# Performance work log

Measured on AMD Instinct MI355X. Metric: run time of the kernel, lower is better.

## Reference

```python
import jax, jax.numpy as jnp
import numpy as np

FEATS = 768
HEAD = 12
HD = FEATS // HEAD  # 64
B, N = 128, 197


def setup_inputs() -> dict:
    key = jax.random.key(0)
    k0, k1, k2 = jax.random.split(key, 3)
    x = jax.random.normal(k0, (B, N, FEATS), dtype=jnp.float32)
    W_qkv = jax.random.normal(k1, (HEAD, HD, 3 * HD), dtype=jnp.float32) * 0.05
    b_qkv = jnp.zeros((HEAD, 3 * HD), dtype=jnp.float32)
    # out_dim_3dk: Linear(feats -> feats)
    W_out = jax.random.normal(k2, (FEATS, FEATS), dtype=jnp.float32) * 0.02
    b_out = jnp.zeros((FEATS,), dtype=jnp.float32)
    return {"x": x, "W_qkv": W_qkv, "b_qkv": b_qkv, "W_out": W_out, "b_out": b_out}


def reference(x, W_qkv, b_qkv, W_out, b_out):
    b, n, f = x.shape
    h, hd = W_qkv.shape[0], W_qkv.shape[1]
    # x.chunk(head, dim=2) == reshape into per-head feature slices
    xh = x.reshape(b, n, h, hd)
    # per-head Linear(hd -> 3*hd): hX_dim_3dk
    qkv = jnp.einsum('bnhd,hde->bnhe', xh, W_qkv) + b_qkv  # [b,n,h,3*hd]
    q, k, v = jnp.split(qkv, 3, axis=-1)  # each [b,n,h,hd]
    # NOTE: original scales by sqrt(feats), not sqrt(head_dim)
    scale = jnp.asarray(f, x.dtype) ** 0.5
    scores = jnp.einsum('bihd,bjhd->bhij', q, k) / scale  # [b,h,n,n]
    p = jax.nn.softmax(scores, axis=-1)
    attn = jnp.einsum('bhij,bjhd->bihd', p, v)  # [b,n,h,hd]
    # concat head outputs along feature dim, then out_dim_3dk
    out = attn.reshape(b, n, f) @ W_out + b_out
    return out  # dropout p=0.0 is identity
```

## Files before the change

### kernel.cpp

```cpp
#include <hip/hip_runtime.h>
#include <hip/hip_bf16.h>

#define FEATS 768
#define HEADS 12
#define HD    64
#define BB    128
#define NN    197
#define M_TOT (BB * NN)
#define SCALE_INV (3.6084391824351615e-02f)
#define VS    216

typedef __bf16 bf16x8 __attribute__((ext_vector_type(8)));
typedef float  f32x4  __attribute__((ext_vector_type(4)));
typedef unsigned short u16x8 __attribute__((ext_vector_type(8)));

__device__ __forceinline__ unsigned short f2bf1(float f) {
    __bf16 h = (__bf16)f;
    return *(unsigned short*)&h;
}
__device__ __forceinline__ unsigned int f2bf2(float lo, float hi) {
    return (unsigned int)f2bf1(lo) | ((unsigned int)f2bf1(hi) << 16);
}

__global__ __launch_bounds__(256) void wqkvt_kernel(
    const float* __restrict__ Wqkv, unsigned short* __restrict__ Wt_sw)
{
    __shared__ float wl[64 * 192];
    const int t = threadIdx.x, h = blockIdx.x;
    const float* Wh = Wqkv + (long)h * (64 * 192);
    for (int i = t; i < 64 * 192; i += 256) wl[i] = Wh[i];
    __syncthreads();
    for (int c = t; c < 1536; c += 256) {
        int row = c >> 3, kc = (c & 7) ^ (row & 7);
        u16x8 v;
        #pragma unroll
        for (int j = 0; j < 8; ++j) v[j] = f2bf1(wl[(kc * 8 + j) * 192 + row]);
        *(u16x8*)&Wt_sw[(long)h * 12288 + c * 8] = v;
    }
}

__global__ __launch_bounds__(512, 4) void qkv_attn_fused(
    const float* __restrict__ x, const unsigned short* __restrict__ Wt_sw,
    const float* __restrict__ bqkv, unsigned short* __restrict__ attn)
{
    __shared__ __align__(16) char lds[80912];
    unsigned short* As  = (unsigned short*)lds;
    unsigned short* Ws  = (unsigned short*)(lds + 26624);
    unsigned short* Ql  = (unsigned short*)lds;
    unsigned short* Kl  = (unsigned short*)(lds + 26624);
    unsigned short* Vtl = (unsigned short*)(lds + 53248);
    unsigned short* Pl  = (unsigned short*)lds;

    const int t  = threadIdx.x;
    const int w  = t >> 6, l = t & 63;
    const int lr = l & 15, g = l >> 4, g4 = g * 4;
    const int b  = blockIdx.x, h = blockIdx.y;

    {
        const uint4 z = {0, 0, 0, 0};
        #pragma unroll
        for (int it = 0; it < 4; ++it) {
            int idx = it * 512 + t;
            if (idx < 1729) *(uint4*)&Vtl[idx * 8] = z;
        }
    }
    #pragma unroll
    for (int it = 0; it < 4; ++it) {
        int p = it * 512 + t;
        if (p < 1664) {
            int row = p >> 3, kc = (p & 7) ^ (row & 7);
            uint4 pk = {0, 0, 0, 0};
            if (row < NN) {
                const float* src = x + ((long)b * NN + row) * FEATS + h * HD + kc * 8;
                const float4 x0 = *(const float4*)src;
                const float4 x1 = *(const float4*)(src + 4);
                pk.x = f2bf2(x0.x, x0.y); pk.y = f2bf2(x0.z, x0.w);
                pk.z = f2bf2(x1.x, x1.y); pk.w = f2bf2(x1.z, x1.w);
            }
            *(uint4*)&As[p * 8] = pk;
        }
    }
    const unsigned short* Wh = Wt_sw + (long)h * 12288;
    #pragma unroll
    for (int it = 0; it < 3; ++it) {
        const int cb = it * 512 + w * 64;
        __builtin_amdgcn_global_load_lds(
            (const __attribute__((address_space(1))) void*)(Wh + (cb + l) * 8),
            (__attribute__((address_space(3))) void*)(Ws + cb * 8),
            16, 0, 0);
    }
    __syncthreads();

    const int wn0 = (w & 3) * 48;
    const int f0  = (w >> 2) * 7;
    const int nf_ = (w >> 2) ? 6 : 7;

    bf16x8 bfr[3][2];
    #pragma unroll
    for (int ni = 0; ni < 3; ++ni) {
        const int rn = wn0 + ni * 16 + lr;
        #pragma unroll
        for (int ks = 0; ks < 2; ++ks)
            bfr[ni][ks] = *(const bf16x8*)&Ws[(rn * 8 + ((ks * 4 + g) ^ (rn & 7))) * 8];
    }

    f32x4 acc[7][3];
    #pragma unroll
    for (int ni = 0; ni < 3; ++ni) {
        const int e0 = wn0 + ni * 16;
        if (e0 < 128) {
            const f32x4 bq = *(const f32x4*)&bqkv[h * 192 + e0 + g4];
            #pragma unroll
            for (int mi = 0; mi < 7; ++mi) acc[mi][ni] = bq;
        } else {
            const float bq = bqkv[h * 192 + e0 + lr];
            #pragma unroll
            for (int mi = 0; mi < 7; ++mi)
                #pragma unroll
                for (int r = 0; r < 4; ++r) acc[mi][ni][r] = bq;
        }
    }

    #pragma unroll
    for (int mi = 0; mi < 7; ++mi) {
        if (mi < nf_) {
            const int rA = (f0 + mi) * 16 + lr;
            bf16x8 a0 = *(const bf16x8*)&As[(rA * 8 + ((0 + g) ^ (rA & 7))) * 8];
            bf16x8 a1 = *(const bf16x8*)&As[(rA * 8 + ((4 + g) ^ (rA & 7))) * 8];
            #pragma unroll
            for (int ni = 0; ni < 3; ++ni) {
                const int e0 = wn0 + ni * 16;
                if (e0 < 128) {
                    acc[mi][ni] = __builtin_amdgcn_mfma_f32_16x16x32_bf16(
                        bfr[ni][0], a0, acc[mi][ni], 0, 0, 0);
                    acc[mi][ni] = __builtin_amdgcn_mfma_f32_16x16x32_bf16(
                        bfr[ni][1], a1, acc[mi][ni], 0, 0, 0);
                } else {
                    acc[mi][ni] = __builtin_amdgcn_mfma_f32_16x16x32_bf16(
                        a0, bfr[ni][0], acc[mi][ni], 0, 0, 0);
                    acc[mi][ni] = __builtin_amdgcn_mfma_f32_16x16x32_bf16(
                        a1, bfr[ni][1], acc[mi][ni], 0, 0, 0);
                }
            }
        }
    }
    __syncthreads();

    #pragma unroll
    for (int mi = 0; mi < 7; ++mi) {
        if (mi < nf_) {
            const int m = (f0 + mi) * 16 + lr;
            #pragma unroll
            for (int ni = 0; ni < 3; ++ni) {
                const int e0 = wn0 + ni * 16;
                uint2 pv;
                pv.x = f2bf2(acc[mi][ni][0], acc[mi][ni][1]);
                pv.y = f2bf2(acc[mi][ni][2], acc[mi][ni][3]);
                if (e0 < 64) {
                    const int c = ((e0 + g4) >> 3) ^ (m & 7);
                    *(uint2*)&Ql[(m * 8 + c) * 8 + (g4 & 7)] = pv;
                } else if (e0 < 128) {
                    const int e = e0 - 64 + g4;
                    const int c = (e >> 3) ^ (m & 7);
                    *(uint2*)&Kl[(m * 8 + c) * 8 + (g4 & 7)] = pv;
                } else {
                    const int d = e0 - 128 + lr;
                    const int n0 = (f0 + mi) * 16 + g4;
                    *(uint2*)&Vtl[d * VS + n0] = pv;
                }
            }
        }
    }
    __syncthreads();

    const int nm = (w < 5) ? 2 : 1;
    bf16x8 qf[2][2];
    #pragma unroll
    for (int mi = 0; mi < 2; ++mi) {
        if (mi == 0 || mi < nm) {
            const int lm = (w + mi * 8) * 16 + lr;
            #pragma unroll
            for (int ks = 0; ks < 2; ++ks)
                qf[mi][ks] = *(const bf16x8*)&Ql[(lm * 8 + ((ks * 4 + g) ^ (lm & 7))) * 8];
        }
    }
    __syncthreads();

    u16x8 ob;
    #pragma unroll
    for (int j = 0; j < 8; ++j) ob[j] = 0x3F80;
    bf16x8 onesf = *(bf16x8*)&ob;

    f32x4 oacc[2][4] = {};
    f32x4 ssum[2] = {};

    for (int tt = 0; tt < 7; ++tt) {
        const int kv0 = tt * 32;
        const int NF2 = (tt == 6) ? 1 : 2;

        bf16x8 kf[2][2];
        #pragma unroll
        for (int nf2 = 0; nf2 < 2; ++nf2) {
            if (nf2 < NF2) {
                const int row = kv0 + nf2 * 16 + lr;
                #pragma unroll
                for (int ks = 0; ks < 2; ++ks)
                    kf[nf2][ks] = *(const bf16x8*)&Kl[(row * 8 + ((ks * 4 + g) ^ (row & 7))) * 8];
            }
        }

        f32x4 s[2][2] = {};
        #pragma unroll
        for (int mi = 0; mi < 2; ++mi) {
            if (mi < nm) {
                #pragma unroll
                for (int nf2 = 0; nf2 < 2; ++nf2) {
                    if (nf2 < NF2) {
                        s[mi][nf2] = __builtin_amdgcn_mfma_f32_16x16x32_bf16(
                            qf[mi][0], kf[nf2][0], s[mi][nf2], 0, 0, 0);
                        s[mi][nf2] = __builtin_amdgcn_mfma_f32_16x16x32_bf16(
                            qf[mi][1], kf[nf2][1], s[mi][nf2], 0, 0, 0);
                    }
                }
            }
        }

        #pragma unroll
        for (int mi = 0; mi < 2; ++mi) {
            if (mi < nm) {
                #pragma unroll
                for (int nf2 = 0; nf2 < 2; ++nf2) {
                    const bool valid = (kv0 + nf2 * 16 + lr) < NN;
                    const int c = nf2 * 2 + (lr >> 3);
                    #pragma unroll
                    for (int r = 0; r < 4; ++r) {
                        float p = __expf(s[mi][nf2][r] * SCALE_INV);
                        p = valid ? p : 0.f;
                        const int q = (w + mi * 8) * 16 + g4 + r;
                        Pl[q * 40 + (c ^ g) * 8 + (lr & 7)] = f2bf1(p);
                    }
                }
            }
        }

        bf16x8 vf[4];
        #pragma unroll
        for (int df = 0; df < 4; ++df)
            vf[df] = *(const bf16x8*)&Vtl[(df * 16 + lr) * VS + kv0 + g * 8];
        #pragma unroll
        for (int mi = 0; mi < 2; ++mi) {
            if (mi < nm) {
                const int q = (w + mi * 8) * 16 + lr;
                bf16x8 pa = *(const bf16x8*)&Pl[q * 40 + (g ^ ((lr >> 2) & 3)) * 8];
                #pragma unroll
                for (int df = 0; df < 4; ++df)
                    oacc[mi][df] = __builtin_amdgcn_mfma_f32_16x16x32_bf16(
                        pa, vf[df], oacc[mi][df], 0, 0, 0);
                ssum[mi] = __builtin_amdgcn_mfma_f32_16x16x32_bf16(
                    pa, onesf, ssum[mi], 0, 0, 0);
            }
        }
    }

    #pragma unroll
    for (int mi = 0; mi < 2; ++mi) {
        if (mi < nm) {
            f32x4 inv;
            #pragma unroll
            for (int r = 0; r < 4; ++r) inv[r] = 1.0f / ssum[mi][r];
            #pragma unroll
            for (int df = 0; df < 4; ++df) {
                #pragma unroll
                for (int r = 0; r < 4; ++r) {
                    const int grow = (w + mi * 8) * 16 + g4 + r;
                    if (grow < NN)
                        attn[((long)b * NN + grow) * FEATS + h * HD + df * 16 + lr]
                            = f2bf1(oacc[mi][df][r] * inv[r]);
                }
            }
        }
    }
}

__global__ __launch_bounds__(256) void wtrans_kernel(
    const float* __restrict__ W, unsigned short* __restrict__ Wt)
{
    __shared__ float tile[32][33];
    const int t  = threadIdx.x;
    const int tx = t & 31, ty = t >> 5;
    const int kb = blockIdx.x * 32, nb = blockIdx.y * 32;
    for (int r = ty; r < 32; r += 8)
        tile[r][tx] = W[(long)(kb + r) * FEATS + nb + tx];
    __syncthreads();
    for (int r = ty; r < 32; r += 8)
        Wt[(long)(nb + r) * FEATS + kb + tx] = f2bf1(tile[tx][r]);
}

__global__ __launch_bounds__(256) void outproj_mfma(
    const unsigned short* __restrict__ A,
    const unsigned short* __restrict__ Bt,
    const float* __restrict__ bout, float* __restrict__ out)
{
    __shared__ unsigned short As[128 * 32];
    __shared__ unsigned short Bs[128 * 32];

    const int t  = threadIdx.x;
    const int w  = t >> 6;
    const int l  = t & 63;
    const int idx  = blockIdx.x;
    const int xcd  = idx & 7, qq = idx >> 3;
    const int start = (xcd < 6) ? xcd * 148 : 888 + (xcd - 6) * 147;
    const int wk = start + qq;
    const int m0 = (wk / 6) * 128;
    const int n0 = (wk % 6) * 128;
    const int wm = (w >> 1) * 64;
    const int wn = (w & 1) * 64;
    const int lr = l & 15;
    const int lk = l >> 4;

    f32x4 acc[4][4] = {};

    for (int k0 = 0; k0 < FEATS; k0 += 32) {
        #pragma unroll
        for (int c = 0; c < 2; ++c) {
            const int off = c * 4096 + t * 16;
            const int row = off >> 6;
            const int col = (off & 63) >> 1;
            const unsigned short* gA = A  + (long)(m0 + row) * FEATS + k0 + col;
            const unsigned short* gB = Bt + (long)(n0 + row) * FEATS + k0 + col;
            __builtin_amdgcn_global_load_lds(
                (const __attribute__((address_space(1))) void*)gA,
                (__attribute__((address_space(3))) void*)(As + c * 2048 + w * 512),
                16, 0, 0);
            __builtin_amdgcn_global_load_lds(
                (const __attribute__((address_space(1))) void*)gB,
                (__attribute__((address_space(3))) void*)(Bs + c * 2048 + w * 512),
                16, 0, 0);
        }
        __syncthreads();

        bf16x8 af[4], bfr[4];
        #pragma unroll
        for (int mi = 0; mi < 4; ++mi)
            af[mi] = *(const bf16x8*)(As + (wm + mi * 16 + lr) * 32 + lk * 8);
        #pragma unroll
        for (int ni = 0; ni < 4; ++ni)
            bfr[ni] = *(const bf16x8*)(Bs + (wn + ni * 16 + lr) * 32 + lk * 8);
        #pragma unroll
        for (int mi = 0; mi < 4; ++mi)
            #pragma unroll
            for (int ni = 0; ni < 4; ++ni)
                acc[mi][ni] = __builtin_amdgcn_mfma_f32_16x16x32_bf16(
                    af[mi], bfr[ni], acc[mi][ni], 0, 0, 0);
        __syncthreads();
    }

    float bv[4];
    #pragma unroll
    for (int ni = 0; ni < 4; ++ni) bv[ni] = bout[n0 + wn + ni * 16 + lr];
    #pragma unroll
    for (int mi = 0; mi < 4; ++mi) {
        #pragma unroll
        for (int ni = 0; ni < 4; ++ni) {
            const int gcol = n0 + wn + ni * 16 + lr;
            #pragma unroll
            for (int r = 0; r < 4; ++r) {
                const int grow = m0 + wm + mi * 16 + lk * 4 + r;
                out[(long)grow * FEATS + gcol] = acc[mi][ni][r] + bv[ni];
            }
        }
    }
}

extern "C" void kernel_launch(void* const* d_in, const int* in_sizes, int n_in,
                              void* d_out, int out_size, void* d_ws, size_t ws_size,
                              hipStream_t stream)
{
    const float* x    = (const float*)d_in[0];
    const float* Wqkv = (const float*)d_in[1];
    const float* bqkv = (const float*)d_in[2];
    const float* Wout = (const float*)d_in[3];
    const float* bout = (const float*)d_in[4];
    float* out = (float*)d_out;

    unsigned short* wsp = (unsigned short*)d_ws;
    const long S = (long)M_TOT * FEATS;
    unsigned short* attn  = wsp;
    unsigned short* Wt_sw = wsp + S;
    unsigned short* Wt    = wsp + S + 150000;

    wqkvt_kernel<<<dim3(HEADS), 256, 0, stream>>>(Wqkv, Wt_sw);

    qkv_attn_fused<<<dim3(BB, HEADS), 512, 0, stream>>>(x, Wt_sw, bqkv, attn);

    wtrans_kernel<<<dim3(FEATS / 32, FEATS / 32), 256, 0, stream>>>(Wout, Wt);

    outproj_mfma<<<dim3(1182), 256, 0, stream>>>(attn, Wt, bout, out);
}
```

Baseline: 119.9 us.

## Swizzle attn and Wout layouts, widen out-proj K tile, merge prep kernels

The attention kernel now writes its bf16 output with an XOR-swizzled 8-element chunk order per row, and the Wout transpose writes the same swizzle. This lets the output projection load 64-wide K tiles straight into LDS with global_load_lds and read them without bank conflicts. The out-proj K step doubles from 32 to 64, halving the number of barriers per tile at the cost of twice the LDS. The two weight-prep kernels are merged into one launch, removing a kernel launch.

Result: no change. 121.0 us (+0.9%).

```diff
diff --git a/kernel.cpp b/kernel.cpp
--- a/kernel.cpp
+++ b/kernel.cpp
@@ -22,20 +22,39 @@
     return (unsigned int)f2bf1(lo) | ((unsigned int)f2bf1(hi) << 16);
 }
 
-__global__ __launch_bounds__(256) void wqkvt_kernel(
-    const float* __restrict__ Wqkv, unsigned short* __restrict__ Wt_sw)
+__global__ __launch_bounds__(256) void prep_kernel(
+    const float* __restrict__ Wqkv, unsigned short* __restrict__ Wt_sw,
+    const float* __restrict__ W,    unsigned short* __restrict__ Wt)
 {
-    __shared__ float wl[64 * 192];
-    const int t = threadIdx.x, h = blockIdx.x;
-    const float* Wh = Wqkv + (long)h * (64 * 192);
-    for (int i = t; i < 64 * 192; i += 256) wl[i] = Wh[i];
-    __syncthreads();
-    for (int c = t; c < 1536; c += 256) {
-        int row = c >> 3, kc = (c & 7) ^ (row & 7);
-        u16x8 v;
-        #pragma unroll
-        for (int j = 0; j < 8; ++j) v[j] = f2bf1(wl[(kc * 8 + j) * 192 + row]);
-        *(u16x8*)&Wt_sw[(long)h * 12288 + c * 8] = v;
+    __shared__ __align__(16) char plds[49152];
+    const int t = threadIdx.x;
+    if (blockIdx.x < 12) {
+        float* wl = (float*)plds;
+        const int h = blockIdx.x;
+        const float* Wh = Wqkv + (long)h * (64 * 192);
+        for (int i = t; i < 64 * 192; i += 256) wl[i] = Wh[i];
+        __syncthreads();
+        for (int c = t; c < 1536; c += 256) {
+            int row = c >> 3, kc = (c & 7) ^ (row & 7);
+            u16x8 v;
+            #pragma unroll
+            for (int j = 0; j < 8; ++j) v[j] = f2bf1(wl[(kc * 8 + j) * 192 + row]);
+            *(u16x8*)&Wt_sw[(long)h * 12288 + c * 8] = v;
+        }
+    } else {
+        float (*tile)[33] = (float(*)[33])plds;
+        const int idx = blockIdx.x - 12;
+        const int kb = (idx % 24) * 32, nb = (idx / 24) * 32;
+        const int tx = t & 31, ty = t >> 5;
+        for (int r = ty; r < 32; r += 8)
+            tile[r][tx] = W[(long)(kb + r) * FEATS + nb + tx];
+        __syncthreads();
+        for (int r = ty; r < 32; r += 8) {
+            const int n = nb + r, k = kb + tx;
+            const long phys = (long)n * FEATS + ((k >> 6) << 6)
+                            + ((((k >> 3) & 7) ^ (n & 7)) << 3) + (k & 7);
+            Wt[phys] = f2bf1(tile[tx][r]);
+        }
     }
 }
 
@@ -273,27 +292,16 @@
                 #pragma unroll
                 for (int r = 0; r < 4; ++r) {
                     const int grow = (w + mi * 8) * 16 + g4 + r;
-                    if (grow < NN)
-                        attn[((long)b * NN + grow) * FEATS + h * HD + df * 16 + lr]
+                    if (grow < NN) {
+                        const long am = (long)b * NN + grow;
+                        const int cc = (df * 2 + (lr >> 3)) ^ ((int)(am & 7));
+                        attn[am * FEATS + h * HD + cc * 8 + (lr & 7)]
                             = f2bf1(oacc[mi][df][r] * inv[r]);
+                    }
                 }
             }
         }
     }
-}
-
-__global__ __launch_bounds__(256) void wtrans_kernel(
-    const float* __restrict__ W, unsigned short* __restrict__ Wt)
-{
-    __shared__ float tile[32][33];
-    const int t  = threadIdx.x;
-    const int tx = t & 31, ty = t >> 5;
-    const int kb = blockIdx.x * 32, nb = blockIdx.y * 32;
-    for (int r = ty; r < 32; r += 8)
-        tile[r][tx] = W[(long)(kb + r) * FEATS + nb + tx];
-    __syncthreads();
-    for (int r = ty; r < 32; r += 8)
-        Wt[(long)(nb + r) * FEATS + kb + tx] = f2bf1(tile[tx][r]);
 }
 
 __global__ __launch_bounds__(256) void outproj_mfma(
@@ -301,8 +309,8 @@
     const unsigned short* __restrict__ Bt,
     const float* __restrict__ bout, float* __restrict__ out)
 {
-    __shared__ unsigned short As[128 * 32];
-    __shared__ unsigned short Bs[128 * 32];
+    __shared__ unsigned short As2[128 * 64];
+    __shared__ unsigned short Bs2[128 * 64];
 
     const int t  = threadIdx.x;
     const int w  = t >> 6;
@@ -317,41 +325,47 @@
     const int wn = (w & 1) * 64;
     const int lr = l & 15;
     const int lk = l >> 4;
+    const int l7 = lr & 7;
 
     f32x4 acc[4][4] = {};
 
-    for (int k0 = 0; k0 < FEATS; k0 += 32) {
-        #pragma unroll
-        for (int c = 0; c < 2; ++c) {
-            const int off = c * 4096 + t * 16;
-            const int row = off >> 6;
-            const int col = (off & 63) >> 1;
-            const unsigned short* gA = A  + (long)(m0 + row) * FEATS + k0 + col;
-            const unsigned short* gB = Bt + (long)(n0 + row) * FEATS + k0 + col;
+    for (int k0 = 0; k0 < FEATS; k0 += 64) {
+        #pragma unroll
+        for (int c = 0; c < 4; ++c) {
+            const int p   = c * 256 + t;
+            const int row = p >> 3;
+            const int col = (p & 7) * 8;
             __builtin_amdgcn_global_load_lds(
-                (const __attribute__((address_space(1))) void*)gA,
-                (__attribute__((address_space(3))) void*)(As + c * 2048 + w * 512),
+                (const __attribute__((address_space(1))) void*)
+                    (A + (long)(m0 + row) * FEATS + k0 + col),
+                (__attribute__((address_space(3))) void*)(As2 + (c * 256 + w * 64) * 8),
                 16, 0, 0);
             __builtin_amdgcn_global_load_lds(
-                (const __attribute__((address_space(1))) void*)gB,
-                (__attribute__((address_space(3))) void*)(Bs + c * 2048 + w * 512),
+                (const __attribute__((address_space(1))) void*)
+                    (Bt + (long)(n0 + row) * FEATS + k0 + col),
+                (__attribute__((address_space(3))) void*)(Bs2 + (c * 256 + w * 64) * 8),
                 16, 0, 0);
         }
         __syncthreads();
 
-        bf16x8 af[4], bfr[4];
-        #pragma unroll
-        for (int mi = 0; mi < 4; ++mi)
-            af[mi] = *(const bf16x8*)(As + (wm + mi * 16 + lr) * 32 + lk * 8);
-        #pragma unroll
-        for (int ni = 0; ni < 4; ++ni)
-            bfr[ni] = *(const bf16x8*)(Bs + (wn + ni * 16 + lr) * 32 + lk * 8);
-        #pragma unroll
-        for (int mi = 0; mi < 4; ++mi)
+        #pragma unroll
+        for (int s = 0; s < 2; ++s) {
+            bf16x8 af[4], bfr[4];
+            #pragma unroll
+            for (int mi = 0; mi < 4; ++mi)
+                af[mi] = *(const bf16x8*)(As2 + (wm + mi * 16 + lr) * 64
+                                              + (((s * 4 + lk) ^ l7)) * 8);
             #pragma unroll
             for (int ni = 0; ni < 4; ++ni)
-                acc[mi][ni] = __builtin_amdgcn_mfma_f32_16x16x32_bf16(
-                    af[mi], bfr[ni], acc[mi][ni], 0, 0, 0);
+                bfr[ni] = *(const bf16x8*)(Bs2 + (wn + ni * 16 + lr) * 64
+                                               + (((s * 4 + lk) ^ l7)) * 8);
+            #pragma unroll
+            for (int mi = 0; mi < 4; ++mi)
+                #pragma unroll
+                for (int ni = 0; ni < 4; ++ni)
+                    acc[mi][ni] = __builtin_amdgcn_mfma_f32_16x16x32_bf16(
+                        af[mi], bfr[ni], acc[mi][ni], 0, 0, 0);
+        }
         __syncthreads();
     }
 
@@ -389,11 +403,9 @@
     unsigned short* Wt_sw = wsp + S;
     unsigned short* Wt    = wsp + S + 150000;
 
-    wqkvt_kernel<<<dim3(HEADS), 256, 0, stream>>>(Wqkv, Wt_sw);
+    prep_kernel<<<dim3(588), 256, 0, stream>>>(Wqkv, Wt_sw, Wout, Wt);
 
     qkv_attn_fused<<<dim3(BB, HEADS), 512, 0, stream>>>(x, Wt_sw, bqkv, attn);
 
-    wtrans_kernel<<<dim3(FEATS / 32, FEATS / 32), 256, 0, stream>>>(Wout, Wt);
-
     outproj_mfma<<<dim3(1182), 256, 0, stream>>>(attn, Wt, bout, out);
 }
```
